# Optimization experiments

Measured on AMD Instinct MI355X. Metric: run time of the kernel, lower is better.

## Reference

```python
import jax, jax.numpy as jnp
import numpy as np

SHARP = 50.0  # softness of the analytic brush edge


def _rasterize(param, dec, ps):
    # param: [N,12], dec: [N] float 0/1 -> fg,[N,3,ps,ps] (color*alpha*dec), alpha [N,3,ps,ps]
    p = jax.nn.sigmoid(param[:, :8])
    x0, y0 = p[:, 0], p[:, 1]
    wd = jnp.maximum(p[:, 2], 1e-2)
    ht = jnp.maximum(p[:, 3], 1e-2)
    theta = p[:, 4] * jnp.pi
    color = p[:, 5:8]
    lin = (jnp.arange(ps, dtype=param.dtype) + 0.5) / ps
    gy, gx = jnp.meshgrid(lin, lin, indexing='ij')            # [ps,ps]
    dx = gx[None] - x0[:, None, None]
    dy = gy[None] - y0[:, None, None]
    ct = jnp.cos(theta)[:, None, None]
    st = jnp.sin(theta)[:, None, None]
    u = dx * ct + dy * st
    v = -dx * st + dy * ct
    alpha = (jax.nn.sigmoid(SHARP * (wd[:, None, None] / 2 - jnp.abs(u)))
             * jax.nn.sigmoid(SHARP * (ht[:, None, None] / 2 - jnp.abs(v))))
    alpha = alpha * dec[:, None, None]                         # masked scatter == multiply
    alpha3 = jnp.broadcast_to(alpha[:, None], (alpha.shape[0], 3, ps, ps))
    fg = color[:, :, None, None] * alpha3                      # foreground*alpha pre-fused
    return fg, alpha3


def reference(param, decision, cur_canvas):
    b, h, w, s, _ = param.shape
    H, W = cur_canvas.shape[-2], cur_canvas.shape[-1]
    ps = 2 * H // h  # patch_size (== 2*W//w)
    dec = decision.astype(cur_canvas.dtype).reshape(-1)
    fg, al = _rasterize(param.reshape(-1, 12), dec, ps)
    fg = fg.reshape(b, h, w, s, 3, ps, ps)
    al = al.reshape(b, h, w, s, 3, ps, ps)
    q = ps // 4
    canvas = jnp.pad(cur_canvas, ((0, 0), (0, 0), (q, q), (q, q)))
    ey, ex = np.arange(0, h, 2), np.arange(0, w, 2)
    oy, ox = np.arange(1, h, 2), np.arange(1, w, 2)

    def blend(cv, rows, cols, off_y, off_x):
        ny, nx = len(rows), len(cols)
        region = cv[:, :, off_y:off_y + ny * ps, off_x:off_x + nx * ps]
        tiles = region.reshape(b, 3, ny, ps, nx, ps).transpose(0, 2, 4, 1, 3, 5)  # [b,ny,nx,3,ps,ps]
        sf = fg[:, rows][:, :, cols]   # [b,ny,nx,s,3,ps,ps]
        sa = al[:, rows][:, :, cols]
        for i in range(s):
            tiles = sf[:, :, :, i] + tiles * (1.0 - sa[:, :, :, i])
        region = tiles.transpose(0, 3, 1, 4, 2, 5).reshape(b, 3, ny * ps, nx * ps)
        return cv.at[:, :, off_y:off_y + ny * ps, off_x:off_x + nx * ps].set(region)

    canvas = blend(canvas, ey, ex, 0, 0)
    canvas = blend(canvas, oy, ox, ps // 2, ps // 2)
    canvas = blend(canvas, oy, ex, ps // 2, 0)
    canvas = blend(canvas, ey, ox, 0, ps // 2)
    return canvas[:, :, q:-q, q:-q]


def setup_inputs() -> dict:
    key = jax.random.key(0)
    k1, k2, k3 = jax.random.split(key, 3)
    b, h, w, s = 1, 64, 64, 5
    H = W = 1024
    param = jax.random.normal(k1, (b, h, w, s, 12), dtype=jnp.float32)
    decision = jax.random.randint(k2, (b, h, w, s), 0, 2, dtype=jnp.int32)
    cur_canvas = jax.random.uniform(k3, (b, 3, H, W), dtype=jnp.float32)
    return {'param': param, 'decision': decision, 'cur_canvas': cur_canvas}
```

## Files before the change

### kernel.cpp

```cpp
#include <hip/hip_runtime.h>

#define PI_F 3.14159265358979323846f
constexpr float SL = 50.0f * 1.44269504089f;

__device__ __forceinline__ float fexp2(float x) {
#if __has_builtin(__builtin_amdgcn_exp2f)
  return __builtin_amdgcn_exp2f(x);
#else
  return __expf(x * 0.69314718056f);
#endif
}
__device__ __forceinline__ float frcp(float x) {
#if __has_builtin(__builtin_amdgcn_rcpf)
  return __builtin_amdgcn_rcpf(x);
#else
  return 1.0f / x;
#endif
}
__device__ __forceinline__ float fsig(float x) {
  return frcp(1.0f + fexp2(-x * 1.44269504089f));
}

__global__ __launch_bounds__(64) void render_kernel(
    const float* __restrict__ param, const int* __restrict__ dec,
    const float* __restrict__ canvas, float* __restrict__ out) {
  __shared__ float4 lds4[20 * 3];

  const int A = blockIdx.y, B = blockIdx.x;
  const int re = (A & 1) ? A - 1 : A;
  const int ro = (A & 1) ? A : A - 1;
  const int ce = (B & 1) ? B - 1 : B;
  const int co = (B & 1) ? B : B - 1;

  const int j = threadIdx.x;

  bool live = false;
  float4 w0q, w1q, w2q;
  if (j < 20) {
    const int k = j / 5;
    const int i = j - k * 5;
    const int rr = (k == 0 || k == 3) ? re : ro;
    const int cc = (k & 1) ? co : ce;
    if ((unsigned)rr < 64u && (unsigned)cc < 64u) {
      const int tid = rr * 64 + cc;
      const int sid = tid * 5 + i;
      if (dec[sid] != 0) {
        const float4* p4 = (const float4*)(param + (size_t)sid * 12);
        float4 a = p4[0];
        float4 b = p4[1];
        float x0 = fsig(a.x), y0 = fsig(a.y);
        float wd = fmaxf(fsig(a.z), 0.01f);
        float ht = fmaxf(fsig(a.w), 0.01f);
        float th = fsig(b.x) * PI_F;
        float ct = __cosf(th), st = __sinf(th);
        w0q = make_float4((float)(cc * 16) + 32.0f * x0,
                          (float)(rr * 16) + 32.0f * y0,
                          ct * (SL / 32.0f), st * (SL / 32.0f));
        w1q = make_float4(SL * wd * 0.5f, SL * ht * 0.5f,
                          fsig(b.y), fsig(b.z));
        w2q = make_float4(fsig(b.w), 0.0f, 0.0f, 0.0f);
        live = true;
      }
    }
  }
  const unsigned long long mask = __ballot(live);
  const int total = __popcll(mask);
  if (live) {
    const int off = __popcll(mask & ((1ull << j) - 1));
    lds4[off * 3 + 0] = w0q;
    lds4[off * 3 + 1] = w1q;
    lds4[off * 3 + 2] = w2q;
  }
  __syncthreads();

  const int cg = j & 3;
  const int row = j >> 2;
  const int Xb = B * 16 - 8 + cg * 4;
  const int Yr = A * 16 - 8 + row;
  const bool valid = ((unsigned)Xb < 1024u) & ((unsigned)Yr < 1024u);
  if (!valid) return;

  const size_t pix = (size_t)Yr * 1024 + Xb;
  float4 v0 = *(const float4*)(canvas + pix);
  float4 v1 = *(const float4*)(canvas + pix + 1024 * 1024);
  float4 v2 = *(const float4*)(canvas + pix + 2 * 1024 * 1024);

  const float fx0 = (float)(B * 16 + cg * 4) + 0.5f;
  const float fy  = (float)(A * 16 + row) + 0.5f;

  for (int s = 0; s < total; ++s) {
    const float4 qa = lds4[s * 3 + 0];
    const float4 qb = lds4[s * 3 + 1];
    const float4 qc = lds4[s * 3 + 2];
    const float dx0 = fx0 - qa.x;
    const float dy  = fy - qa.y;
    float u = dx0 * qa.z + dy * qa.w;
    float w = dy * qa.z - dx0 * qa.w;
    float* pv0 = &v0.x;
    float* pv1 = &v1.x;
    float* pv2 = &v2.x;
#pragma unroll
    for (int m = 0; m < 4; ++m) {
      const float e1 = fexp2(fabsf(u) - qb.x);
      const float e2 = fexp2(fabsf(w) - qb.y);
      const float al = frcp((1.0f + e1) * (1.0f + e2));
      pv0[m] = fmaf(al, qb.z - pv0[m], pv0[m]);
      pv1[m] = fmaf(al, qb.w - pv1[m], pv1[m]);
      pv2[m] = fmaf(al, qc.x - pv2[m], pv2[m]);
      u += qa.z;
      w -= qa.w;
    }
  }

  *(float4*)(out + pix) = v0;
  *(float4*)(out + pix + 1024 * 1024) = v1;
  *(float4*)(out + pix + 2 * 1024 * 1024) = v2;
}

extern "C" void kernel_launch(void* const* d_in, const int* in_sizes, int n_in,
                              void* d_out, int out_size, void* d_ws, size_t ws_size,
                              hipStream_t stream) {
  const float* param  = (const float*)d_in[0];
  const int*   dec    = (const int*)d_in[1];
  const float* canvas = (const float*)d_in[2];
  float* outp = (float*)d_out;
  (void)d_ws; (void)ws_size;

  dim3 grid(65, 65, 1);
  render_kernel<<<grid, 64, 0, stream>>>(param, dec, canvas, outp);
}
```

Baseline: 79.39 us.

## Pack four tiles per block and issue canvas loads before parameter setup

Each block now holds four independent wavefronts, one per 16x16 tile, each with its own LDS slot, so there are fewer tiny blocks to launch. The __syncthreads is dropped because each wave only reads what it wrote itself. Canvas loads move ahead of the sigmoid/trig parameter decoding so their memory latency overlaps that setup. Out-of-range threads now load from index 0 and skip the store instead of returning early. The grid is 33x33, so some waves are idle.

```diff
diff --git a/kernel.cpp b/kernel.cpp
--- a/kernel.cpp
+++ b/kernel.cpp
@@ -21,18 +21,32 @@
   return frcp(1.0f + fexp2(-x * 1.44269504089f));
 }
 
-__global__ __launch_bounds__(64) void render_kernel(
+__global__ __launch_bounds__(256) void render_kernel(
     const float* __restrict__ param, const int* __restrict__ dec,
     const float* __restrict__ canvas, float* __restrict__ out) {
-  __shared__ float4 lds4[20 * 3];
+  __shared__ float4 lds4[4][20 * 3];
 
-  const int A = blockIdx.y, B = blockIdx.x;
+  const int t = threadIdx.x;
+  const int wv = t >> 6;
+  const int j  = t & 63;
+  const int A = blockIdx.y * 2 + (wv >> 1);
+  const int B = blockIdx.x * 2 + (wv & 1);
+  if (A > 64 || B > 64) return;
+
+  const int cg = j & 3;
+  const int row = j >> 2;
+  const int Xb = B * 16 - 8 + cg * 4;
+  const int Yr = A * 16 - 8 + row;
+  const bool valid = ((unsigned)Xb < 1024u) & ((unsigned)Yr < 1024u);
+  const size_t pix = valid ? ((size_t)Yr * 1024 + Xb) : 0;
+  float4 v0 = *(const float4*)(canvas + pix);
+  float4 v1 = *(const float4*)(canvas + pix + 1024 * 1024);
+  float4 v2 = *(const float4*)(canvas + pix + 2 * 1024 * 1024);
+
   const int re = (A & 1) ? A - 1 : A;
   const int ro = (A & 1) ? A : A - 1;
   const int ce = (B & 1) ? B - 1 : B;
   const int co = (B & 1) ? B : B - 1;
-
-  const int j = threadIdx.x;
 
   bool live = false;
   float4 w0q, w1q, w2q;
@@ -42,8 +56,7 @@
     const int rr = (k == 0 || k == 3) ? re : ro;
     const int cc = (k & 1) ? co : ce;
     if ((unsigned)rr < 64u && (unsigned)cc < 64u) {
-      const int tid = rr * 64 + cc;
-      const int sid = tid * 5 + i;
+      const int sid = (rr * 64 + cc) * 5 + i;
       if (dec[sid] != 0) {
         const float4* p4 = (const float4*)(param + (size_t)sid * 12);
         float4 a = p4[0];
@@ -67,31 +80,18 @@
   const int total = __popcll(mask);
   if (live) {
     const int off = __popcll(mask & ((1ull << j) - 1));
-    lds4[off * 3 + 0] = w0q;
-    lds4[off * 3 + 1] = w1q;
-    lds4[off * 3 + 2] = w2q;
+    lds4[wv][off * 3 + 0] = w0q;
+    lds4[wv][off * 3 + 1] = w1q;
+    lds4[wv][off * 3 + 2] = w2q;
   }
-  __syncthreads();
-
-  const int cg = j & 3;
-  const int row = j >> 2;
-  const int Xb = B * 16 - 8 + cg * 4;
-  const int Yr = A * 16 - 8 + row;
-  const bool valid = ((unsigned)Xb < 1024u) & ((unsigned)Yr < 1024u);
-  if (!valid) return;
-
-  const size_t pix = (size_t)Yr * 1024 + Xb;
-  float4 v0 = *(const float4*)(canvas + pix);
-  float4 v1 = *(const float4*)(canvas + pix + 1024 * 1024);
-  float4 v2 = *(const float4*)(canvas + pix + 2 * 1024 * 1024);
 
   const float fx0 = (float)(B * 16 + cg * 4) + 0.5f;
   const float fy  = (float)(A * 16 + row) + 0.5f;
 
   for (int s = 0; s < total; ++s) {
-    const float4 qa = lds4[s * 3 + 0];
-    const float4 qb = lds4[s * 3 + 1];
-    const float4 qc = lds4[s * 3 + 2];
+    const float4 qa = lds4[wv][s * 3 + 0];
+    const float4 qb = lds4[wv][s * 3 + 1];
+    const float4 qc = lds4[wv][s * 3 + 2];
     const float dx0 = fx0 - qa.x;
     const float dy  = fy - qa.y;
     float u = dx0 * qa.z + dy * qa.w;
@@ -112,9 +112,11 @@
     }
   }
 
-  *(float4*)(out + pix) = v0;
-  *(float4*)(out + pix + 1024 * 1024) = v1;
-  *(float4*)(out + pix + 2 * 1024 * 1024) = v2;
+  if (valid) {
+    *(float4*)(out + pix) = v0;
+    *(float4*)(out + pix + 1024 * 1024) = v1;
+    *(float4*)(out + pix + 2 * 1024 * 1024) = v2;
+  }
 }
 
 extern "C" void kernel_launch(void* const* d_in, const int* in_sizes, int n_in,
@@ -126,6 +128,6 @@
   float* outp = (float*)d_out;
   (void)d_ws; (void)ws_size;
 
-  dim3 grid(65, 65, 1);
-  render_kernel<<<grid, 64, 0, stream>>>(param, dec, canvas, outp);
+  dim3 grid(33, 33, 1);
+  render_kernel<<<grid, 256, 0, stream>>>(param, dec, canvas, outp);
 }
```

New measurement: 79.89 us. Within noise of the previous version (+0.6%).
